# Kernel optimization log

Hardware: AMD Instinct MI355X
Metric: run time of the kernel (lower is better)

The kernel has to match this reference:

```python
import jax, jax.numpy as jnp
import numpy as np

N_ENTS = 50000
N_RELS2 = 460  # num_rels * 2
H_DIM = 128
T = 8
E = 200000
M = 400000
RRELU_SLOPE = (1.0 / 8.0 + 1.0 / 3.0) / 2.0  # F.rrelu eval mode
EPS = 1e-12


def l2norm(x):
    # F.normalize(x) along last dim
    return x / jnp.maximum(jnp.linalg.norm(x, axis=-1, keepdims=True), EPS)


def gru_cell(x, h, W_ih, W_hh, b_ih, b_hh):
    # torch.nn.GRUCell math
    gi = x @ W_ih.T + b_ih
    gh = h @ W_hh.T + b_hh
    i_r, i_z, i_n = jnp.split(gi, 3, axis=-1)
    h_r, h_z, h_n = jnp.split(gh, 3, axis=-1)
    r = jax.nn.sigmoid(i_r + h_r)
    z = jax.nn.sigmoid(i_z + h_z)
    n = jnp.tanh(i_n + r * h_n)
    return (1.0 - z) * n + z * h


def rrelu(x):
    return jnp.where(x >= 0, x, RRELU_SLOPE * x)


def setup_inputs() -> dict:
    key = jax.random.key(0)
    ks = jax.random.split(key, 12)
    src = jax.random.randint(ks[0], (T, E), 0, N_ENTS, dtype=jnp.int32)
    dst = jax.random.randint(ks[1], (T, E), 0, N_ENTS, dtype=jnp.int32)
    etype = jax.random.randint(ks[2], (T, E), 0, N_RELS2, dtype=jnp.int32)
    r_to_e_idx = jax.random.randint(ks[3], (T, M), 0, N_ENTS, dtype=jnp.int32)
    rel_seg = jax.random.randint(ks[4], (T, M), 0, N_RELS2, dtype=jnp.int32)
    s = 1.0 / np.sqrt(H_DIM)
    dynamic_emb = jax.random.normal(ks[5], (N_ENTS, H_DIM), jnp.float32)
    emb_rel = jax.random.normal(ks[6], (N_RELS2, H_DIM), jnp.float32) * s
    gru_W_ih = jax.random.uniform(ks[7], (3 * H_DIM, 2 * H_DIM), jnp.float32, -s, s)
    gru_W_hh = jax.random.uniform(ks[8], (3 * H_DIM, H_DIM), jnp.float32, -s, s)
    gru_b_ih = jnp.zeros((3 * H_DIM,), jnp.float32)
    gru_b_hh = jnp.zeros((3 * H_DIM,), jnp.float32)
    rgcn_W = jax.random.normal(ks[9], (2, H_DIM, H_DIM), jnp.float32) * s  # 2 hidden layers
    time_gate_weight = jax.random.normal(ks[10], (H_DIM, H_DIM), jnp.float32) * s
    time_gate_bias = jnp.zeros((H_DIM,), jnp.float32)
    return {
        "src": src, "dst": dst, "etype": etype,
        "r_to_e_idx": r_to_e_idx, "rel_seg": rel_seg,
        "dynamic_emb": dynamic_emb, "emb_rel": emb_rel,
        "gru_W_ih": gru_W_ih, "gru_W_hh": gru_W_hh,
        "gru_b_ih": gru_b_ih, "gru_b_hh": gru_b_hh,
        "rgcn_W": rgcn_W,
        "time_gate_weight": time_gate_weight, "time_gate_bias": time_gate_bias,
    }


def reference(src, dst, etype, r_to_e_idx, rel_seg, dynamic_emb, emb_rel,
              gru_W_ih, gru_W_hh, gru_b_ih, gru_b_hh, rgcn_W,
              time_gate_weight, time_gate_bias):
    h_init = l2norm(dynamic_emb)  # layer_norm=True path

    def step(carry, xs):
        h, h0 = carry
        src_t, dst_t, etype_t, rte_t, rseg_t = xs
        # --- relation evolution: mean of incident entity embeddings per relation ---
        temp_e = h[rte_t]  # [M, d]
        sums = jax.ops.segment_sum(temp_e, rseg_t, num_segments=N_RELS2)
        cnts = jax.ops.segment_sum(jnp.ones((M,), h.dtype), rseg_t, num_segments=N_RELS2)
        x_mean = jnp.where(cnts[:, None] > 0, sums / jnp.maximum(cnts[:, None], 1.0), 0.0)
        x_input = jnp.concatenate([emb_rel, x_mean], axis=1)  # [2R, 2d]
        h0 = l2norm(gru_cell(x_input, h0, gru_W_ih, gru_W_hh, gru_b_ih, gru_b_hh))
        # --- RGCN (UnionRGCNLayer x2): msg=(h[src]+r[etype])@W, sum agg, 1/indeg norm, rrelu ---
        deg = jax.ops.segment_sum(jnp.ones((E,), h.dtype), dst_t, num_segments=N_ENTS)
        norm = jnp.where(deg > 0, 1.0 / jnp.maximum(deg, 1.0), 0.0)  # [N]
        nh = h
        for l in range(2):
            msg = (nh[src_t] + h0[etype_t]) @ rgcn_W[l]  # [E, d]
            agg = jax.ops.segment_sum(msg, dst_t, num_segments=N_ENTS) * norm[:, None]
            nh = rrelu(agg)
        current_h = l2norm(nh)
        # --- time gate fusion ---
        tw = jax.nn.sigmoid(h @ time_gate_weight + time_gate_bias)
        h_new = tw * current_h + (1.0 - tw) * h
        return (h_new, h0), h_new

    (_, h0_final), history = jax.lax.scan(
        step, (h_init, emb_rel), (src, dst, etype, r_to_e_idx, rel_seg))
    return history, h0_final  # [T, N, d], [2R, d]
```

## Files before the change

### kernel.cpp

```cpp
#include <hip/hip_runtime.h>
#include <math.h>

#define NENT 50000
#define NE2 (NENT / 2)
#define NR2 460
#define HD 128
#define TS 8
#define EPC 200000
#define MPC 400000
#define RSLOPE 0.22916666666666666f
#define RBLK 128
#define NTOT (TS * NENT)
#define NB8 ((NTOT + 255) / 256)
#define SCAN2_PER ((NB8 + 255) / 256)

typedef __attribute__((ext_vector_type(8))) short bfrag;
typedef __attribute__((ext_vector_type(4))) float facc;

__device__ __forceinline__ float sigm(float x) { return 1.0f / (1.0f + expf(-x)); }
__device__ __forceinline__ float rrelu_f(float x) { return x >= 0.0f ? x : RSLOPE * x; }
__device__ __forceinline__ unsigned short f2bf_rne(float x) {
  unsigned u = __float_as_uint(x);
  unsigned r = (u + 0x7FFFu + ((u >> 16) & 1u)) >> 16;
  return (unsigned short)r;
}
__device__ __forceinline__ float bf2f(unsigned short b) {
  return __uint_as_float(((unsigned)b) << 16);
}
__device__ __forceinline__ float bfLO(unsigned u) { return __uint_as_float(u << 16); }
__device__ __forceinline__ float bfHI(unsigned u) { return __uint_as_float(u & 0xFFFF0000u); }
__device__ __forceinline__ unsigned packbf(float x, float y) {
  return (unsigned)f2bf_rne(x) | ((unsigned)f2bf_rne(y) << 16);
}

__global__ __launch_bounds__(HD) void k_l2rows(const float* __restrict__ in,
                                               float* __restrict__ out,
                                               unsigned short* __restrict__ out_bf) {
  int r = blockIdx.x, j = threadIdx.x;
  __shared__ float red[HD];
  float v = in[(size_t)r * HD + j];
  red[j] = v * v;
  __syncthreads();
  for (int s = HD / 2; s > 0; s >>= 1) { if (j < s) red[j] += red[j + s]; __syncthreads(); }
  float rn = 1.0f / fmaxf(sqrtf(red[0]), 1e-12f);
  float o = v * rn;
  out[(size_t)r * HD + j] = o;
  out_bf[(size_t)r * HD + j] = f2bf_rne(o);
}

__global__ void k_hist(const int* __restrict__ idx, int* __restrict__ cnt,
                       int n, int per_t, int stride) {
  int i = blockIdx.x * blockDim.x + threadIdx.x;
  int gs = gridDim.x * blockDim.x;
  for (; i < n; i += gs) atomicAdd(&cnt[(i / per_t) * stride + idx[i]], 1);
}

__global__ __launch_bounds__(256) void k_histR2(const int* __restrict__ rseg,
                                                int* __restrict__ blkcnt) {
  __shared__ int h[NR2];
  int b = blockIdx.x, t = blockIdx.y, tid = threadIdx.x;
  for (int i = tid; i < NR2; i += 256) h[i] = 0;
  __syncthreads();
  const int* rs = rseg + (size_t)t * MPC;
  int chunk = (MPC + RBLK - 1) / RBLK;
  int m0 = b * chunk, m1 = min(MPC, m0 + chunk);
  for (int m = m0 + tid; m < m1; m += 256) atomicAdd(&h[rs[m]], 1);
  __syncthreads();
  for (int i = tid; i < NR2; i += 256) blkcnt[((size_t)(t * RBLK + b)) * NR2 + i] = h[i];
}

__global__ __launch_bounds__(256) void k_scanR2a(const int* __restrict__ blkcnt,
                                                 int* __restrict__ tot) {
  int idx = blockIdx.x * 256 + threadIdx.x;
  if (idx >= TS * NR2) return;
  int t = idx / NR2, r = idx - t * NR2;
  int s = 0;
  for (int b = 0; b < RBLK; ++b) s += blkcnt[((size_t)(t * RBLK + b)) * NR2 + r];
  tot[idx] = s;
}

__global__ __launch_bounds__(512) void k_scanR2b(const int* __restrict__ tot,
    int* __restrict__ offsR, float* __restrict__ invc) {
  __shared__ int s[TS * NR2];
  int tid = threadIdx.x;
  for (int i = tid; i < TS * NR2; i += 512) s[i] = tot[i];
  __syncthreads();
  if (tid < TS) {
    int acc = tid * MPC;
    for (int r = 0; r < NR2; ++r) { int c = s[tid * NR2 + r]; s[tid * NR2 + r] = acc; acc += c; }
  }
  __syncthreads();
  for (int i = tid; i < TS * NR2; i += 512) {
    offsR[i] = s[i];
    int c = tot[i];
    invc[i] = c > 0 ? 1.0f / (float)c : 0.0f;
  }
  if (tid == 0) offsR[TS * NR2] = TS * MPC;
}

__global__ __launch_bounds__(256) void k_scanR2c(int* __restrict__ blkcnt,
                                                 const int* __restrict__ offsR) {
  int gw = (blockIdx.x * blockDim.x + threadIdx.x) >> 6;
  int lane = threadIdx.x & 63;
  if (gw >= TS * NR2) return;
  int t = gw / NR2, r = gw - t * NR2;
  size_t i0 = ((size_t)(t * RBLK + lane * 2)) * NR2 + r;
  size_t i1 = ((size_t)(t * RBLK + lane * 2 + 1)) * NR2 + r;
  int v0 = blkcnt[i0], v1 = blkcnt[i1];
  int s = v0 + v1;
  int sc = s;
  #pragma unroll
  for (int o = 1; o < 64; o <<= 1) {
    int x = __shfl_up(sc, o, 64);
    if (lane >= o) sc += x;
  }
  int basev = offsR[gw] + (sc - s);
  blkcnt[i0] = basev;
  blkcnt[i1] = basev + v0;
}

__global__ __launch_bounds__(256) void k_scatterR2(const int* __restrict__ rte,
    const int* __restrict__ rseg, const int* __restrict__ blkbase,
    int* __restrict__ out) {
  __shared__ int cur[NR2];
  int b = blockIdx.x, t = blockIdx.y, tid = threadIdx.x;
  for (int i = tid; i < NR2; i += 256) cur[i] = blkbase[((size_t)(t * RBLK + b)) * NR2 + i];
  __syncthreads();
  const int* rs = rseg + (size_t)t * MPC;
  const int* re = rte + (size_t)t * MPC;
  int chunk = (MPC + RBLK - 1) / RBLK;
  int m0 = b * chunk, m1 = min(MPC, m0 + chunk);
  for (int m = m0 + tid; m < m1; m += 256) {
    int r = rs[m];
    int p = atomicAdd(&cur[r], 1);
    out[p] = re[m];
  }
}

__global__ __launch_bounds__(256) void k_scan1(const int* __restrict__ deg,
    int* __restrict__ offs, float* __restrict__ normv, int* __restrict__ bsum) {
  __shared__ int sd[256];
  int b = blockIdx.x, tid = threadIdx.x;
  int i = b * 256 + tid;
  int v = (i < NTOT) ? deg[i] : 0;
  sd[tid] = v;
  __syncthreads();
  for (int o = 1; o < 256; o <<= 1) {
    int x = (tid >= o) ? sd[tid - o] : 0;
    __syncthreads();
    sd[tid] += x;
    __syncthreads();
  }
  if (i < NTOT) {
    offs[i] = sd[tid] - v;
    normv[i] = v > 0 ? 1.0f / (float)v : 0.0f;
  }
  if (tid == 255) bsum[b] = sd[255];
}

__global__ __launch_bounds__(256) void k_scan2(int* __restrict__ bsum) {
  __shared__ int part[256];
  int tid = threadIdx.x;
  int base = tid * SCAN2_PER;
  int local[SCAN2_PER];
  int s = 0;
  #pragma unroll
  for (int k = 0; k < SCAN2_PER; ++k) {
    int v = (base + k < NB8) ? bsum[base + k] : 0;
    local[k] = s;
    s += v;
  }
  part[tid] = s;
  __syncthreads();
  for (int o = 1; o < 256; o <<= 1) {
    int x = (tid >= o) ? part[tid - o] : 0;
    __syncthreads();
    part[tid] += x;
    __syncthreads();
  }
  int pre = (tid > 0) ? part[tid - 1] : 0;
  #pragma unroll
  for (int k = 0; k < SCAN2_PER; ++k)
    if (base + k < NB8) bsum[base + k] = pre + local[k];
}

__global__ __launch_bounds__(256) void k_scan3(int* __restrict__ offs, int* __restrict__ cur,
                                               const int* __restrict__ bsum) {
  int b = blockIdx.x;
  int i = b * 256 + threadIdx.x;
  if (i < NTOT) {
    int o = offs[i] + bsum[b];
    offs[i] = o;
    cur[i] = o;
  }
  if (b == 0 && threadIdx.x == 0) offs[NTOT] = TS * EPC;
}

__global__ void k_scatterE(const int* __restrict__ src, const int* __restrict__ dst,
                           const int* __restrict__ ety, int* __restrict__ cur,
                           unsigned* __restrict__ se) {
  int tid0 = blockIdx.x * blockDim.x + threadIdx.x;
  int gs = gridDim.x * blockDim.x;
  for (int t = 0; t < TS; ++t) {
    const int* s = src + (size_t)t * EPC;
    const int* d = dst + (size_t)t * EPC;
    const int* e = ety + (size_t)t * EPC;
    int* ct = cur + t * NENT;
    for (int i = tid0; i < EPC; i += gs) {
      int dd = d[i];
      int p = atomicAdd(&ct[dd], 1);
      se[p] = ((unsigned)s[i] << 9) | (unsigned)e[i];
    }
  }
}

__global__ __launch_bounds__(256) void k_prepW(const float* __restrict__ W,
    unsigned short* __restrict__ hi, unsigned short* __restrict__ lo) {
  int t = blockIdx.x * 256 + threadIdx.x;
  int nt = t >> 8, ks = (t >> 6) & 3, lane = t & 63;
  int n = nt * 16 + (lane & 15);
  int k0 = ks * 32 + ((lane >> 4) << 3);
  #pragma unroll
  for (int j = 0; j < 8; ++j) {
    float v = W[(k0 + j) * HD + n];
    unsigned short h = f2bf_rne(v);
    hi[t * 8 + j] = h;
    lo[t * 8 + j] = f2bf_rne(v - bf2f(h));
  }
}

__global__ __launch_bounds__(512) void k_relgru(
    const unsigned short* __restrict__ h_bf,
    const int* __restrict__ offs, const int* __restrict__ rte_csr,
    const float* __restrict__ invcnt,
    const float* __restrict__ emb_rel, const float* __restrict__ h0s,
    const float* __restrict__ Wih, const float* __restrict__ Whh,
    const float* __restrict__ bih, const float* __restrict__ bhh,
    float* __restrict__ h0d, unsigned short* __restrict__ h0d_bf) {
  int rel = blockIdx.x;
  int tid = threadIdx.x;
  int w = __builtin_amdgcn_readfirstlane(tid >> 6);
  int lane = tid & 63;
  int o0 = offs[rel], o1 = offs[rel + 1];
  int n = o1 - o0;
  int s0 = o0 + ((n * w) >> 3);
  int s1 = o0 + ((n * (w + 1)) >> 3);
  const unsigned* h4 = (const unsigned*)h_bf;
  float sx = 0.f, sy = 0.f;
  int p = s0;
  for (; p + 4 <= s1; p += 4) {
    int i0 = rte_csr[p], i1 = rte_csr[p + 1], i2 = rte_csr[p + 2], i3 = rte_csr[p + 3];
    unsigned u0 = h4[(size_t)i0 * 64 + lane];
    unsigned u1 = h4[(size_t)i1 * 64 + lane];
    unsigned u2 = h4[(size_t)i2 * 64 + lane];
    unsigned u3 = h4[(size_t)i3 * 64 + lane];
    sx += (bfLO(u0) + bfLO(u1)) + (bfLO(u2) + bfLO(u3));
    sy += (bfHI(u0) + bfHI(u1)) + (bfHI(u2) + bfHI(u3));
  }
  for (; p < s1; ++p) {
    unsigned u0 = h4[(size_t)rte_csr[p] * 64 + lane];
    sx += bfLO(u0);
    sy += bfHI(u0);
  }
  __shared__ float red[8][HD];
  red[w][lane * 2] = sx;
  red[w][lane * 2 + 1] = sy;
  __syncthreads();
  __shared__ __align__(16) float xr[2 * HD];
  __shared__ __align__(16) float hh[HD];
  __shared__ float red2[HD];
  float hv0 = 0.f;
  if (tid < HD) {
    int j = tid;
    float inv = invcnt[rel];
    float xm = 0.f;
    #pragma unroll
    for (int sp = 0; sp < 8; ++sp) xm += red[sp][j];
    xr[j] = emb_rel[rel * HD + j];
    xr[HD + j] = xm * inv;
    hv0 = h0s[rel * HD + j];
    hh[j] = hv0;
  }
  __syncthreads();
  float hv = 0.f;
  if (tid < HD) {
    int j = tid;
    float gr = bih[j], gz = bih[HD + j], gn = bih[2 * HD + j];
    const float4* W4 = (const float4*)Wih;
    int rowA = j * 64, rowB = (j + HD) * 64, rowC = (j + 2 * HD) * 64;
    #pragma unroll 4
    for (int k4 = 0; k4 < 64; ++k4) {
      float4 xa = ((const float4*)xr)[k4];
      float4 w0 = W4[rowA + k4];
      float4 w1 = W4[rowB + k4];
      float4 w2 = W4[rowC + k4];
      gr += w0.x * xa.x + w0.y * xa.y + w0.z * xa.z + w0.w * xa.w;
      gz += w1.x * xa.x + w1.y * xa.y + w1.z * xa.z + w1.w * xa.w;
      gn += w2.x * xa.x + w2.y * xa.y + w2.z * xa.z + w2.w * xa.w;
    }
    float hr = bhh[j], hz = bhh[HD + j], hn = bhh[2 * HD + j];
    const float4* Wh4 = (const float4*)Whh;
    int rA = j * 32, rB = (j + HD) * 32, rC = (j + 2 * HD) * 32;
    #pragma unroll 4
    for (int k4 = 0; k4 < 32; ++k4) {
      float4 xa = ((const float4*)hh)[k4];
      float4 w0 = Wh4[rA + k4];
      float4 w1 = Wh4[rB + k4];
      float4 w2 = Wh4[rC + k4];
      hr += w0.x * xa.x + w0.y * xa.y + w0.z * xa.z + w0.w * xa.w;
      hz += w1.x * xa.x + w1.y * xa.y + w1.z * xa.z + w1.w * xa.w;
      hn += w2.x * xa.x + w2.y * xa.y + w2.z * xa.z + w2.w * xa.w;
    }
    float rg = sigm(gr + hr);
    float zg = sigm(gz + hz);
    float ng = tanhf(gn + rg * hn);
    hv = (1.0f - zg) * ng + zg * hv0;
    red2[tid] = hv * hv;
  }
  __syncthreads();
  for (int s = HD / 2; s > 0; s >>= 1) {
    if (tid < s) red2[tid] += red2[tid + s];
    __syncthreads();
  }
  if (tid < HD) {
    float rn = 1.0f / fmaxf(sqrtf(red2[0]), 1e-12f);
    float o = hv * rn;
    h0d[rel * HD + tid] = o;
    h0d_bf[rel * HD + tid] = f2bf_rne(o);
  }
}

template<int PASS>
__global__ __launch_bounds__(256) void k_edge2(
    const unsigned short* __restrict__ nh_bf, const unsigned short* __restrict__ h0_bf,
    const int* __restrict__ offs, const unsigned* __restrict__ se,
    const float* __restrict__ norm, unsigned* __restrict__ Tbf,
    float* __restrict__ agg) {
  int gw = __builtin_amdgcn_readfirstlane((blockIdx.x * blockDim.x + threadIdx.x) >> 6);
  int lane = threadIdx.x & 63;
  if (gw >= NE2) return;
  int rA = gw, rB = gw + NE2;
  int a0 = offs[rA], a1 = offs[rA + 1];
  int b0 = offs[rB], b1 = offs[rB + 1];
  const unsigned* nh4 = (const unsigned*)nh_bf;
  const unsigned* h04 = (const unsigned*)h0_bf;
  float nax = 0.f, nay = 0.f, tax = 0.f, tay = 0.f;
  float nbx = 0.f, nby = 0.f, tbx = 0.f, tby = 0.f;
  int pa = a0, pb = b0;
  for (; pa + 4 <= a1 && pb + 4 <= b1; pa += 4, pb += 4) {
    unsigned e0 = se[pa], e1 = se[pa + 1], e2 = se[pa + 2], e3 = se[pa + 3];
    unsigned f0 = se[pb], f1 = se[pb + 1], f2 = se[pb + 2], f3 = se[pb + 3];
    unsigned ua = nh4[(size_t)(e0 >> 9) * 64 + lane];
    unsigned ub = nh4[(size_t)(e1 >> 9) * 64 + lane];
    unsigned uc = nh4[(size_t)(e2 >> 9) * 64 + lane];
    unsigned ud = nh4[(size_t)(e3 >> 9) * 64 + lane];
    unsigned va = nh4[(size_t)(f0 >> 9) * 64 + lane];
    unsigned vb = nh4[(size_t)(f1 >> 9) * 64 + lane];
    unsigned vc = nh4[(size_t)(f2 >> 9) * 64 + lane];
    unsigned vd = nh4[(size_t)(f3 >> 9) * 64 + lane];
    nax += (bfLO(ua) + bfLO(ub)) + (bfLO(uc) + bfLO(ud));
    nay += (bfHI(ua) + bfHI(ub)) + (bfHI(uc) + bfHI(ud));
    nbx += (bfLO(va) + bfLO(vb)) + (bfLO(vc) + bfLO(vd));
    nby += (bfHI(va) + bfHI(vb)) + (bfHI(vc) + bfHI(vd));
    if (PASS == 1) {
      unsigned ha = h04[(size_t)(e0 & 511u) * 64 + lane];
      unsigned hb = h04[(size_t)(e1 & 511u) * 64 + lane];
      unsigned hc = h04[(size_t)(e2 & 511u) * 64 + lane];
      unsigned hd = h04[(size_t)(e3 & 511u) * 64 + lane];
      unsigned ga = h04[(size_t)(f0 & 511u) * 64 + lane];
      unsigned gb = h04[(size_t)(f1 & 511u) * 64 + lane];
      unsigned gc = h04[(size_t)(f2 & 511u) * 64 + lane];
      unsigned gd = h04[(size_t)(f3 & 511u) * 64 + lane];
      tax += (bfLO(ha) + bfLO(hb)) + (bfLO(hc) + bfLO(hd));
      tay += (bfHI(ha) + bfHI(hb)) + (bfHI(hc) + bfHI(hd));
      tbx += (bfLO(ga) + bfLO(gb)) + (bfLO(gc) + bfLO(gd));
      tby += (bfHI(ga) + bfHI(gb)) + (bfHI(gc) + bfHI(gd));
    }
  }
  for (; pa < a1; ++pa) {
    unsigned e0 = se[pa];
    unsigned ua = nh4[(size_t)(e0 >> 9) * 64 + lane];
    nax += bfLO(ua);
    nay += bfHI(ua);
    if (PASS == 1) {
      unsigned ha = h04[(size_t)(e0 & 511u) * 64 + lane];
      tax += bfLO(ha);
      tay += bfHI(ha);
    }
  }
  for (; pb < b1; ++pb) {
    unsigned f0 = se[pb];
    unsigned va = nh4[(size_t)(f0 >> 9) * 64 + lane];
    nbx += bfLO(va);
    nby += bfHI(va);
    if (PASS == 1) {
      unsigned ga = h04[(size_t)(f0 & 511u) * 64 + lane];
      tbx += bfLO(ga);
      tby += bfHI(ga);
    }
  }
  float nma = norm[rA], nmb = norm[rB];
  if (PASS == 1) {
    Tbf[(size_t)rA * 64 + lane] = packbf(tax, tay);
    Tbf[(size_t)rB * 64 + lane] = packbf(tbx, tby);
    ((float2*)agg)[(size_t)rA * 64 + lane] = make_float2((nax + tax) * nma, (nay + tay) * nma);
    ((float2*)agg)[(size_t)rB * 64 + lane] = make_float2((nbx + tbx) * nmb, (nby + tby) * nmb);
  } else {
    unsigned tva = Tbf[(size_t)rA * 64 + lane];
    unsigned tvb = Tbf[(size_t)rB * 64 + lane];
    ((float2*)agg)[(size_t)rA * 64 + lane] =
        make_float2((nax + bfLO(tva)) * nma, (nay + bfHI(tva)) * nma);
    ((float2*)agg)[(size_t)rB * 64 + lane] =
        make_float2((nbx + bfLO(tvb)) * nmb, (nby + bfHI(tvb)) * nmb);
  }
}

__device__ __forceinline__ void stage_rows(const float* __restrict__ A, int base, int nrows,
                                           unsigned short* AsH, unsigned short* AsL,
                                           int tid) {
  const float4* A4 = (const float4*)A;
  #pragma unroll
  for (int it = 0; it < 8; ++it) {
    int idx = tid + it * 256;
    int r = idx >> 5, c4 = idx & 31;
    int c0 = c4 * 4;
    float4 v = make_float4(0.f, 0.f, 0.f, 0.f);
    if (base + r < nrows) v = A4[(size_t)(base + r) * 32 + c4];
    int chunk = (c0 >> 3) ^ (r & 7);
    int p = r * 128 + chunk * 8 + (c0 & 7);
    unsigned short h0 = f2bf_rne(v.x), h1 = f2bf_rne(v.y);
    unsigned short h2 = f2bf_rne(v.z), h3 = f2bf_rne(v.w);
    ushort4 hv; hv.x = h0; hv.y = h1; hv.z = h2; hv.w = h3;
    *(ushort4*)&AsH[p] = hv;
    ushort4 lv;
    lv.x = f2bf_rne(v.x - bf2f(h0)); lv.y = f2bf_rne(v.y - bf2f(h1));
    lv.z = f2bf_rne(v.z - bf2f(h2)); lv.w = f2bf_rne(v.w - bf2f(h3));
    *(ushort4*)&AsL[p] = lv;
  }
}

__device__ __forceinline__ void mfma_128(const unsigned short* AsH, const unsigned short* AsL,
                                         const unsigned short* __restrict__ wHi,
                                         const unsigned short* __restrict__ wLo,
                                         int w, int lane, facc* acc) {
  int lrow = lane & 15;
  int arow = w * 16 + lrow;
  #pragma unroll
  for (int ks = 0; ks < 4; ++ks) {
    int chunk = (ks * 4 + (lane >> 4)) ^ (arow & 7);
    int p = arow * 128 + chunk * 8;
    bfrag aH = *(const bfrag*)&AsH[p];
    bfrag aL = *(const bfrag*)&AsL[p];
    #pragma unroll
    for (int nt = 0; nt < 8; ++nt) {
      int fi = ((nt * 4 + ks) * 64 + lane) * 8;
      bfrag bH = *(const bfrag*)&wHi[fi];
      bfrag bL = *(const bfrag*)&wLo[fi];
      acc[nt] = __builtin_amdgcn_mfma_f32_16x16x32_bf16(aH, bH, acc[nt], 0, 0, 0);
      acc[nt] = __builtin_amdgcn_mfma_f32_16x16x32_bf16(aH, bL, acc[nt], 0, 0, 0);
      acc[nt] = __builtin_amdgcn_mfma_f32_16x16x32_bf16(aL, bH, acc[nt], 0, 0, 0);
    }
  }
}

__global__ __launch_bounds__(256) void k_mm1(
    const float* __restrict__ A, unsigned short* __restrict__ Abf,
    const unsigned short* __restrict__ wHi, const unsigned short* __restrict__ wLo,
    int nrows) {
  __shared__ __align__(16) unsigned short AsH[64 * 128];
  __shared__ __align__(16) unsigned short AsL[64 * 128];
  int tid = threadIdx.x;
  int base = blockIdx.x * 64;
  stage_rows(A, base, nrows, AsH, AsL, tid);
  __syncthreads();
  int w = tid >> 6, lane = tid & 63;
  int lrow = lane & 15, lk = lane >> 4;
  facc acc[8];
  #pragma unroll
  for (int nt = 0; nt < 8; ++nt) acc[nt] = (facc){0.f, 0.f, 0.f, 0.f};
  mfma_128(AsH, AsL, wHi, wLo, w, lane, acc);
  #pragma unroll
  for (int nt = 0; nt < 8; ++nt)
    #pragma unroll
    for (int r = 0; r < 4; ++r) {
      int row = base + w * 16 + lk * 4 + r;
      if (row < nrows) Abf[(size_t)row * HD + nt * 16 + lrow] = f2bf_rne(rrelu_f(acc[nt][r]));
    }
}

__global__ __launch_bounds__(256) void k_mm2_final(
    const float* __restrict__ A, const float* __restrict__ Hin,
    float* __restrict__ Hout, unsigned short* __restrict__ Hout_bf,
    const unsigned short* __restrict__ w2Hi, const unsigned short* __restrict__ w2Lo,
    const unsigned short* __restrict__ wtHi, const unsigned short* __restrict__ wtLo,
    const float* __restrict__ bias, int nrows) {
  __shared__ __align__(16) unsigned short AsH[64 * 128];
  __shared__ __align__(16) unsigned short AsL[64 * 128];
  int tid = threadIdx.x;
  int base = blockIdx.x * 64;
  int w = tid >> 6, lane = tid & 63;
  int lrow = lane & 15, lk = lane >> 4;
  stage_rows(A, base, nrows, AsH, AsL, tid);
  __syncthreads();
  facc acc[8];
  #pragma unroll
  for (int nt = 0; nt < 8; ++nt) acc[nt] = (facc){0.f, 0.f, 0.f, 0.f};
  mfma_128(AsH, AsL, w2Hi, w2Lo, w, lane, acc);
  #pragma unroll
  for (int nt = 0; nt < 8; ++nt)
    #pragma unroll
    for (int r = 0; r < 4; ++r) acc[nt][r] = rrelu_f(acc[nt][r]);
  __syncthreads();
  stage_rows(Hin, base, nrows, AsH, AsL, tid);
  __syncthreads();
  facc acc2[8];
  #pragma unroll
  for (int nt = 0; nt < 8; ++nt) acc2[nt] = (facc){0.f, 0.f, 0.f, 0.f};
  mfma_128(AsH, AsL, wtHi, wtLo, w, lane, acc2);
  float ss[4] = {0.f, 0.f, 0.f, 0.f};
  #pragma unroll
  for (int r = 0; r < 4; ++r) {
    #pragma unroll
    for (int nt = 0; nt < 8; ++nt) ss[r] += acc[nt][r] * acc[nt][r];
    #pragma unroll
    for (int o = 1; o < 16; o <<= 1) ss[r] += __shfl_xor(ss[r], o, 64);
    ss[r] = 1.0f / fmaxf(sqrtf(ss[r]), 1e-12f);
  }
  #pragma unroll
  for (int r = 0; r < 4; ++r) {
    int row = base + w * 16 + lk * 4 + r;
    if (row >= nrows) continue;
    #pragma unroll
    for (int nt = 0; nt < 8; ++nt) {
      int col = nt * 16 + lrow;
      float hv = Hin[(size_t)row * HD + col];
      float tw = sigm(acc2[nt][r] + bias[col]);
      float res = tw * (acc[nt][r] * ss[r]) + (1.0f - tw) * hv;
      Hout[(size_t)row * HD + col] = res;
      Hout_bf[(size_t)row * HD + col] = f2bf_rne(res);
    }
  }
}

extern "C" void kernel_launch(void* const* d_in, const int* in_sizes, int n_in,
                              void* d_out, int out_size, void* d_ws, size_t ws_size,
                              hipStream_t stream) {
  const int* src    = (const int*)d_in[0];
  const int* dst    = (const int*)d_in[1];
  const int* etype  = (const int*)d_in[2];
  const int* rte    = (const int*)d_in[3];
  const int* rseg   = (const int*)d_in[4];
  const float* dyn  = (const float*)d_in[5];
  const float* emb_rel = (const float*)d_in[6];
  const float* W_ih = (const float*)d_in[7];
  const float* W_hh = (const float*)d_in[8];
  const float* b_ih = (const float*)d_in[9];
  const float* b_hh = (const float*)d_in[10];
  const float* rgcnW = (const float*)d_in[11];
  const float* tgW  = (const float*)d_in[12];
  const float* tgB  = (const float*)d_in[13];
  float* out = (float*)d_out;
  (void)in_sizes; (void)n_in; (void)out_size; (void)ws_size;

  float* ws = (float*)d_ws;
  size_t off = 0;
  float* agg1    = ws + off; off += (size_t)NENT * HD;
  float* agg2    = ws + off; off += (size_t)NENT * HD;
  float* h0a     = ws + off; off += (size_t)NR2 * HD;
  float* h0b     = ws + off; off += (size_t)NR2 * HD;
  float* normv8  = ws + off; off += NTOT;
  float* invc8   = ws + off; off += TS * NR2;
  off = (off + 3) & ~(size_t)3;
  unsigned* Tbf  = (unsigned*)(ws + off); off += (size_t)NENT * 64;
  unsigned short* h_bf    = (unsigned short*)(ws + off); off += (size_t)NENT * HD / 2;
  unsigned short* agg1_bf = (unsigned short*)(ws + off); off += (size_t)NENT * HD / 2;
  unsigned short* h0abf   = (unsigned short*)(ws + off); off += (size_t)NR2 * HD / 2 + 1;
  unsigned short* h0bbf   = (unsigned short*)(ws + off); off += (size_t)NR2 * HD / 2 + 1;
  unsigned short* wf = (unsigned short*)(ws + off);
  unsigned short* w1H = wf;            unsigned short* w1L = wf + 16384;
  unsigned short* w2H = wf + 32768;    unsigned short* w2L = wf + 49152;
  unsigned short* wtH = wf + 65536;    unsigned short* wtL = wf + 81920;
  off += (6 * 16384) / 2;
  unsigned* csr_se8 = (unsigned*)(ws + off); off += (size_t)TS * EPC;
  int* csr_rte8  = (int*)(ws + off);  off += (size_t)TS * MPC;
  int* degE8     = (int*)(ws + off);  off += NTOT;
  int* offsE8    = (int*)(ws + off);  off += NTOT + 2;
  int* curE8     = (int*)(ws + off);  off += NTOT;
  int* bsum      = (int*)(ws + off);  off += NB8;
  int* blkcntR8  = (int*)(ws + off);  off += (size_t)TS * RBLK * NR2;
  int* offsR8    = (int*)(ws + off);  off += TS * NR2 + 2;
  int* totR      = (int*)(ws + off);  off += TS * NR2;

  hipMemsetAsync(degE8, 0, (size_t)NTOT * sizeof(int), stream);
  k_hist<<<2048, 256, 0, stream>>>(dst, degE8, TS * EPC, EPC, NENT);
  k_scan1<<<NB8, 256, 0, stream>>>(degE8, offsE8, normv8, bsum);
  k_scan2<<<1, 256, 0, stream>>>(bsum);
  k_scan3<<<NB8, 256, 0, stream>>>(offsE8, curE8, bsum);
  k_scatterE<<<1024, 256, 0, stream>>>(src, dst, etype, curE8, csr_se8);
  k_histR2<<<dim3(RBLK, TS), 256, 0, stream>>>(rseg, blkcntR8);
  k_scanR2a<<<(TS * NR2 + 255) / 256, 256, 0, stream>>>(blkcntR8, totR);
  k_scanR2b<<<1, 512, 0, stream>>>(totR, offsR8, invc8);
  k_scanR2c<<<(TS * NR2 * 64 + 255) / 256, 256, 0, stream>>>(blkcntR8, offsR8);
  k_scatterR2<<<dim3(RBLK, TS), 256, 0, stream>>>(rte, rseg, blkcntR8, csr_rte8);
  k_prepW<<<8, 256, 0, stream>>>(rgcnW, w1H, w1L);
  k_prepW<<<8, 256, 0, stream>>>(rgcnW + HD * HD, w2H, w2L);
  k_prepW<<<8, 256, 0, stream>>>(tgW, wtH, wtL);

  k_l2rows<<<NENT, HD, 0, stream>>>(dyn, out, h_bf);

  float* h0bufs[2] = {h0a, h0b};
  unsigned short* h0bfbufs[2] = {h0abf, h0bbf};
  for (int t = 0; t < TS; ++t) {
    const float* h = out + (size_t)(t == 0 ? 0 : (t - 1)) * NENT * HD;
    float* hout = out + (size_t)t * NENT * HD;
    const float* h0s = (t == 0) ? emb_rel : h0bufs[(t - 1) & 1];
    float* h0d = h0bufs[t & 1];
    unsigned short* h0d_bf = h0bfbufs[t & 1];

    k_relgru<<<NR2, 512, 0, stream>>>(h_bf, offsR8 + t * NR2, csr_rte8,
                                      invc8 + t * NR2, emb_rel, h0s,
                                      W_ih, W_hh, b_ih, b_hh, h0d, h0d_bf);

    k_edge2<1><<<(NE2 * 64 + 255) / 256, 256, 0, stream>>>(
        h_bf, h0d_bf, offsE8 + t * NENT, csr_se8, normv8 + t * NENT, Tbf, agg1);
    k_mm1<<<(NENT + 63) / 64, 256, 0, stream>>>(agg1, agg1_bf, w1H, w1L, NENT);
    k_edge2<2><<<(NE2 * 64 + 255) / 256, 256, 0, stream>>>(
        agg1_bf, (const unsigned short*)nullptr, offsE8 + t * NENT, csr_se8,
        normv8 + t * NENT, Tbf, agg2);
    k_mm2_final<<<(NENT + 63) / 64, 256, 0, stream>>>(agg2, h, hout, h_bf,
                                                      w2H, w2L, wtH, wtL, tgB, NENT);
  }
  hipMemcpyAsync(out + (size_t)TS * NENT * HD, h0bufs[(TS - 1) & 1],
                 (size_t)NR2 * HD * sizeof(float), hipMemcpyDeviceToDevice, stream);
}
```

Before: 1.595 ms.

## Split relation mean gather and GRU into separate kernels with wider grid

Splits the per-relation gather-mean and GRU cell into two kernels. The gather now runs on a 2D grid of 460x8 blocks of 256 threads, each writing a partial sum. A second small kernel reduces the partials and computes the GRU with 128 threads per relation. This spreads the memory-bound gather over many more workgroups, so per-block latency and load imbalance matter less. The cost is an extra launch and a round trip of the partials through global memory, both repeated per timestep.

```diff
diff --git a/kernel.cpp b/kernel.cpp
--- a/kernel.cpp
+++ b/kernel.cpp
@@ -13,6 +13,7 @@
 #define NTOT (TS * NENT)
 #define NB8 ((NTOT + 255) / 256)
 #define SCAN2_PER ((NB8 + 255) / 256)
+#define RSP 8
 
 typedef __attribute__((ext_vector_type(8))) short bfrag;
 typedef __attribute__((ext_vector_type(4))) float facc;
@@ -229,27 +230,24 @@
   }
 }
 
-__global__ __launch_bounds__(512) void k_relgru(
-    const unsigned short* __restrict__ h_bf,
+__global__ __launch_bounds__(256) void k_relmean(const unsigned short* __restrict__ h_bf,
     const int* __restrict__ offs, const int* __restrict__ rte_csr,
-    const float* __restrict__ invcnt,
-    const float* __restrict__ emb_rel, const float* __restrict__ h0s,
-    const float* __restrict__ Wih, const float* __restrict__ Whh,
-    const float* __restrict__ bih, const float* __restrict__ bhh,
-    float* __restrict__ h0d, unsigned short* __restrict__ h0d_bf) {
-  int rel = blockIdx.x;
-  int tid = threadIdx.x;
-  int w = __builtin_amdgcn_readfirstlane(tid >> 6);
-  int lane = tid & 63;
+    float* __restrict__ partials) {
+  int rel = blockIdx.x, sp = blockIdx.y;
   int o0 = offs[rel], o1 = offs[rel + 1];
   int n = o1 - o0;
-  int s0 = o0 + ((n * w) >> 3);
-  int s1 = o0 + ((n * (w + 1)) >> 3);
+  int w = __builtin_amdgcn_readfirstlane(threadIdx.x >> 6);
+  int lane = threadIdx.x & 63;
+  int s0 = o0 + ((n * sp) >> 3);
+  int s1 = o0 + ((n * (sp + 1)) >> 3);
   const unsigned* h4 = (const unsigned*)h_bf;
   float sx = 0.f, sy = 0.f;
-  int p = s0;
-  for (; p + 4 <= s1; p += 4) {
-    int i0 = rte_csr[p], i1 = rte_csr[p + 1], i2 = rte_csr[p + 2], i3 = rte_csr[p + 3];
+  int p = s0 + w;
+  for (; p + 12 < s1; p += 16) {
+    int i0 = rte_csr[p];
+    int i1 = rte_csr[p + 4];
+    int i2 = rte_csr[p + 8];
+    int i3 = rte_csr[p + 12];
     unsigned u0 = h4[(size_t)i0 * 64 + lane];
     unsigned u1 = h4[(size_t)i1 * 64 + lane];
     unsigned u2 = h4[(size_t)i2 * 64 + lane];
@@ -257,77 +255,78 @@
     sx += (bfLO(u0) + bfLO(u1)) + (bfLO(u2) + bfLO(u3));
     sy += (bfHI(u0) + bfHI(u1)) + (bfHI(u2) + bfHI(u3));
   }
-  for (; p < s1; ++p) {
+  for (; p < s1; p += 4) {
     unsigned u0 = h4[(size_t)rte_csr[p] * 64 + lane];
     sx += bfLO(u0);
     sy += bfHI(u0);
   }
-  __shared__ float red[8][HD];
+  __shared__ float red[4][HD];
   red[w][lane * 2] = sx;
   red[w][lane * 2 + 1] = sy;
   __syncthreads();
+  if (threadIdx.x < HD) {
+    int j = threadIdx.x;
+    float t = red[0][j] + red[1][j] + red[2][j] + red[3][j];
+    partials[((size_t)sp * NR2 + rel) * HD + j] = t;
+  }
+}
+
+__global__ __launch_bounds__(HD) void k_gru(
+    const float* __restrict__ partials, const float* __restrict__ invcnt,
+    const float* __restrict__ emb_rel, const float* __restrict__ h0s,
+    const float* __restrict__ Wih, const float* __restrict__ Whh,
+    const float* __restrict__ bih, const float* __restrict__ bhh,
+    float* __restrict__ h0d, unsigned short* __restrict__ h0d_bf) {
+  int r = blockIdx.x, j = threadIdx.x;
   __shared__ __align__(16) float xr[2 * HD];
   __shared__ __align__(16) float hh[HD];
-  __shared__ float red2[HD];
-  float hv0 = 0.f;
-  if (tid < HD) {
-    int j = tid;
-    float inv = invcnt[rel];
-    float xm = 0.f;
-    #pragma unroll
-    for (int sp = 0; sp < 8; ++sp) xm += red[sp][j];
-    xr[j] = emb_rel[rel * HD + j];
-    xr[HD + j] = xm * inv;
-    hv0 = h0s[rel * HD + j];
-    hh[j] = hv0;
-  }
-  __syncthreads();
-  float hv = 0.f;
-  if (tid < HD) {
-    int j = tid;
-    float gr = bih[j], gz = bih[HD + j], gn = bih[2 * HD + j];
-    const float4* W4 = (const float4*)Wih;
-    int rowA = j * 64, rowB = (j + HD) * 64, rowC = (j + 2 * HD) * 64;
-    #pragma unroll 4
-    for (int k4 = 0; k4 < 64; ++k4) {
-      float4 xa = ((const float4*)xr)[k4];
-      float4 w0 = W4[rowA + k4];
-      float4 w1 = W4[rowB + k4];
-      float4 w2 = W4[rowC + k4];
-      gr += w0.x * xa.x + w0.y * xa.y + w0.z * xa.z + w0.w * xa.w;
-      gz += w1.x * xa.x + w1.y * xa.y + w1.z * xa.z + w1.w * xa.w;
-      gn += w2.x * xa.x + w2.y * xa.y + w2.z * xa.z + w2.w * xa.w;
-    }
-    float hr = bhh[j], hz = bhh[HD + j], hn = bhh[2 * HD + j];
-    const float4* Wh4 = (const float4*)Whh;
-    int rA = j * 32, rB = (j + HD) * 32, rC = (j + 2 * HD) * 32;
-    #pragma unroll 4
-    for (int k4 = 0; k4 < 32; ++k4) {
-      float4 xa = ((const float4*)hh)[k4];
-      float4 w0 = Wh4[rA + k4];
-      float4 w1 = Wh4[rB + k4];
-      float4 w2 = Wh4[rC + k4];
-      hr += w0.x * xa.x + w0.y * xa.y + w0.z * xa.z + w0.w * xa.w;
-      hz += w1.x * xa.x + w1.y * xa.y + w1.z * xa.z + w1.w * xa.w;
-      hn += w2.x * xa.x + w2.y * xa.y + w2.z * xa.z + w2.w * xa.w;
-    }
-    float rg = sigm(gr + hr);
-    float zg = sigm(gz + hz);
-    float ng = tanhf(gn + rg * hn);
-    hv = (1.0f - zg) * ng + zg * hv0;
-    red2[tid] = hv * hv;
-  }
-  __syncthreads();
-  for (int s = HD / 2; s > 0; s >>= 1) {
-    if (tid < s) red2[tid] += red2[tid + s];
-    __syncthreads();
-  }
-  if (tid < HD) {
-    float rn = 1.0f / fmaxf(sqrtf(red2[0]), 1e-12f);
-    float o = hv * rn;
-    h0d[rel * HD + tid] = o;
-    h0d_bf[rel * HD + tid] = f2bf_rne(o);
-  }
+  __shared__ float red[HD];
+  float inv = invcnt[r];
+  xr[j] = emb_rel[r * HD + j];
+  float xm = 0.f;
+  #pragma unroll
+  for (int sp = 0; sp < RSP; ++sp) xm += partials[((size_t)sp * NR2 + r) * HD + j];
+  xr[HD + j] = xm * inv;
+  float hv0 = h0s[r * HD + j];
+  hh[j] = hv0;
+  __syncthreads();
+  float gr = bih[j], gz = bih[HD + j], gn = bih[2 * HD + j];
+  const float4* W4 = (const float4*)Wih;
+  int rowA = j * 64, rowB = (j + HD) * 64, rowC = (j + 2 * HD) * 64;
+  #pragma unroll 4
+  for (int k4 = 0; k4 < 64; ++k4) {
+    float4 xa = ((const float4*)xr)[k4];
+    float4 w0 = W4[rowA + k4];
+    float4 w1 = W4[rowB + k4];
+    float4 w2 = W4[rowC + k4];
+    gr += w0.x * xa.x + w0.y * xa.y + w0.z * xa.z + w0.w * xa.w;
+    gz += w1.x * xa.x + w1.y * xa.y + w1.z * xa.z + w1.w * xa.w;
+    gn += w2.x * xa.x + w2.y * xa.y + w2.z * xa.z + w2.w * xa.w;
+  }
+  float hr = bhh[j], hz = bhh[HD + j], hn = bhh[2 * HD + j];
+  const float4* Wh4 = (const float4*)Whh;
+  int rA = j * 32, rB = (j + HD) * 32, rC = (j + 2 * HD) * 32;
+  #pragma unroll 4
+  for (int k4 = 0; k4 < 32; ++k4) {
+    float4 xa = ((const float4*)hh)[k4];
+    float4 w0 = Wh4[rA + k4];
+    float4 w1 = Wh4[rB + k4];
+    float4 w2 = Wh4[rC + k4];
+    hr += w0.x * xa.x + w0.y * xa.y + w0.z * xa.z + w0.w * xa.w;
+    hz += w1.x * xa.x + w1.y * xa.y + w1.z * xa.z + w1.w * xa.w;
+    hn += w2.x * xa.x + w2.y * xa.y + w2.z * xa.z + w2.w * xa.w;
+  }
+  float rg = sigm(gr + hr);
+  float zg = sigm(gz + hz);
+  float ng = tanhf(gn + rg * hn);
+  float hv = (1.0f - zg) * ng + zg * hv0;
+  red[j] = hv * hv;
+  __syncthreads();
+  for (int s = HD / 2; s > 0; s >>= 1) { if (j < s) red[j] += red[j + s]; __syncthreads(); }
+  float rn = 1.0f / fmaxf(sqrtf(red[0]), 1e-12f);
+  float o = hv * rn;
+  h0d[r * HD + j] = o;
+  h0d_bf[r * HD + j] = f2bf_rne(o);
 }
 
 template<int PASS>
@@ -566,6 +565,7 @@
   size_t off = 0;
   float* agg1    = ws + off; off += (size_t)NENT * HD;
   float* agg2    = ws + off; off += (size_t)NENT * HD;
+  float* parts   = ws + off; off += (size_t)RSP * NR2 * HD;
   float* h0a     = ws + off; off += (size_t)NR2 * HD;
   float* h0b     = ws + off; off += (size_t)NR2 * HD;
   float* normv8  = ws + off; off += NTOT;
@@ -617,9 +617,9 @@
     float* h0d = h0bufs[t & 1];
     unsigned short* h0d_bf = h0bfbufs[t & 1];
 
-    k_relgru<<<NR2, 512, 0, stream>>>(h_bf, offsR8 + t * NR2, csr_rte8,
-                                      invc8 + t * NR2, emb_rel, h0s,
-                                      W_ih, W_hh, b_ih, b_hh, h0d, h0d_bf);
+    k_relmean<<<dim3(NR2, RSP), 256, 0, stream>>>(h_bf, offsR8 + t * NR2, csr_rte8, parts);
+    k_gru<<<NR2, HD, 0, stream>>>(parts, invc8 + t * NR2, emb_rel, h0s,
+                                  W_ih, W_hh, b_ih, b_hh, h0d, h0d_bf);
 
     k_edge2<1><<<(NE2 * 64 + 255) / 256, 256, 0, stream>>>(
         h_bf, h0d_bf, offsE8 + t * NENT, csr_se8, normv8 + t * NENT, Tbf, agg1);
```

After: 1.589 ms. No clear change (-0.4%).
